# Kernel optimization log

Measured on AMD Instinct MI355X. Metric: run time of the kernel, lower is better.

Reference implementation:

```python
import jax, jax.numpy as jnp
import numpy as np

B, C, W, H = 16, 256, 32, 32  # L = W*H = 1024
NUM_HEAD = 4
DIM_HEAD = C  # dim_head defaults to in_channels


def setup_inputs() -> dict:
    key = jax.random.key(0)
    ks = jax.random.split(key, 6)
    s = 0.02  # small init scale, like trained linear weights
    return {
        "x": jax.random.normal(ks[0], (B, C, W, H), dtype=jnp.float32),
        "Wq": jax.random.normal(ks[1], (NUM_HEAD, DIM_HEAD, C), dtype=jnp.float32) * s,
        "Wk": jax.random.normal(ks[2], (NUM_HEAD, DIM_HEAD, C), dtype=jnp.float32) * s,
        "Wv": jax.random.normal(ks[3], (NUM_HEAD, DIM_HEAD, C), dtype=jnp.float32) * s,
        "Wo_w": jax.random.normal(ks[4], (C, NUM_HEAD * DIM_HEAD), dtype=jnp.float32) * s,
        "Wo_b": jax.random.normal(ks[5], (C,), dtype=jnp.float32) * s,
    }


def reference(x, Wq, Wk, Wv, Wo_w, Wo_b):
    b, c, w, h = x.shape
    L = w * h
    # [b,c,w,h] -> [b,L,c]
    xs = jnp.transpose(x, (0, 2, 3, 1)).reshape(b, L, c)
    # per-head projections (torch Linear: y = x @ W^T), batched over heads
    Q = jnp.einsum('blc,hdc->bhld', xs, Wq)
    K = jnp.einsum('blc,hdc->bhld', xs, Wk)
    V = jnp.einsum('blc,hdc->bhld', xs, Wv)
    # no softmax: scores = Q K^T, heads = scores V
    scores = jnp.einsum('bhld,bhmd->bhlm', Q, K)  # [b,H,L,L]
    heads = jnp.einsum('bhlm,bhmd->bhld', scores, V)  # [b,H,L,d]
    # concat heads along channel dim -> [b,L,H*d], then output projection
    cat = jnp.transpose(heads, (0, 2, 1, 3)).reshape(b, L, -1)
    z = cat @ Wo_w.T + Wo_b  # [b,L,c]
    return jnp.transpose(z, (0, 2, 1)).reshape(b, c, w, h)
```

## Files before the change

kernel.cpp:

```cpp
#include <hip/hip_runtime.h>
#include <hip/hip_bf16.h>

typedef __attribute__((ext_vector_type(8))) short s8v;
typedef __attribute__((ext_vector_type(4))) float f4v;

__device__ inline ushort f2bf(float f) {
    unsigned u = __builtin_bit_cast(unsigned, f);
    unsigned r = (u + 0x7fffu + ((u >> 16) & 1u)) >> 16;
    return (ushort)r;
}

__device__ inline void gload16(const ushort* g, ushort* l) {
    __builtin_amdgcn_global_load_lds(
        (const __attribute__((address_space(1))) unsigned*)g,
        (__attribute__((address_space(3))) unsigned*)l, 16, 0, 0);
}

__global__ __launch_bounds__(256) void kprep(
    const float* __restrict__ x, const float* __restrict__ Wq, const float* __restrict__ Wk,
    const float* __restrict__ Wv, const float* __restrict__ Wo,
    ushort* __restrict__ xb, ushort* __restrict__ xlc,
    ushort* __restrict__ wqT, ushort* __restrict__ wkT, ushort* __restrict__ wvT,
    ushort* __restrict__ wo16) {
    __shared__ __align__(16) ushort t[64][72];
    int j = blockIdx.x, tid = threadIdx.x;
    int r = tid >> 2, c0 = (tid & 3) * 16;
    if (j < 1024) {
        int lt = j & 15, ct = (j >> 4) & 3, b = j >> 6;
        size_t so = ((size_t)(b * 256 + ct * 64 + r)) * 1024 + lt * 64 + c0;
        const float* src = x + so;
        ushort* db = xb + so;
#pragma unroll
        for (int i = 0; i < 16; i += 4) {
            float4 v = *(const float4*)(src + i);
            ushort4 u = { f2bf(v.x), f2bf(v.y), f2bf(v.z), f2bf(v.w) };
            *(ushort4*)(db + i) = u;
            *(ushort4*)(&t[r][c0 + i]) = u;
        }
        __syncthreads();
        ushort* dl = xlc + ((size_t)(b * 1024 + lt * 64 + r)) * 256 + ct * 64 + c0;
#pragma unroll
        for (int i = 0; i < 16; i += 4) {
            ushort4 u = { t[c0 + i][r], t[c0 + i + 1][r], t[c0 + i + 2][r], t[c0 + i + 3][r] };
            *(ushort4*)(dl + i) = u;
        }
    } else if (j < 1216) {
        int q = j - 1024;
        int tile = q & 15, h = (q >> 4) & 3, which = q >> 6;
        const float* src = which == 0 ? Wq : which == 1 ? Wk : Wv;
        ushort* dst = which == 0 ? wqT : which == 1 ? wkT : wvT;
        int tr = tile >> 2, tc = tile & 3;
        const float* s = src + (size_t)h * 65536 + (size_t)(tr * 64 + r) * 256 + tc * 64 + c0;
#pragma unroll
        for (int i = 0; i < 16; i += 4) {
            float4 v = *(const float4*)(s + i);
            ushort4 u = { f2bf(v.x), f2bf(v.y), f2bf(v.z), f2bf(v.w) };
            *(ushort4*)(&t[r][c0 + i]) = u;
        }
        __syncthreads();
        ushort* d = dst + (size_t)h * 65536 + (size_t)(tc * 64 + r) * 256 + tr * 64 + c0;
#pragma unroll
        for (int i = 0; i < 16; i += 4) {
            ushort4 u = { t[c0 + i][r], t[c0 + i + 1][r], t[c0 + i + 2][r], t[c0 + i + 3][r] };
            *(ushort4*)(d + i) = u;
        }
    } else {
        int q = j - 1216;
#pragma unroll
        for (int rr = 0; rr < 4; ++rr) {
            int i = (q * 1024 + rr * 256 + tid) * 4;
            float4 v = *(const float4*)(Wo + i);
            ushort4 u = { f2bf(v.x), f2bf(v.y), f2bf(v.z), f2bf(v.w) };
            *(ushort4*)(wo16 + i) = u;
        }
    }
}


__device__ __forceinline__ void gemm64p(
    const ushort* __restrict__ Xb, const ushort* __restrict__ Yb,
    int ldx, int ldy, ushort* lds, int row0, int col0, int K,
    ushort* __restrict__ O, int ldo) {
    const int tid = threadIdx.x, wave = tid >> 6, lane = tid & 63;
    const int wr = wave >> 1, wc = wave & 1;
    const int rA = lane & 15, kg = lane >> 4;
    const int srow = wave * 16 + (lane >> 2);
    const int scol = ((lane & 3) ^ ((lane >> 3) & 3)) * 8;
    ushort* LA = lds;
    ushort* LB = lds + 8192;
    const int NT = K >> 5;
    f4v acc[2][2] = {};

    const ushort* gx = Xb + (size_t)(row0 + srow) * ldx + scol;
    const ushort* gy = Yb + (size_t)(col0 + srow) * ldy + scol;
    gload16(gx + 0,  LA + 0 * 2048 + wave * 512);
    gload16(gy + 0,  LB + 0 * 2048 + wave * 512);
    gload16(gx + 32, LA + 1 * 2048 + wave * 512);
    gload16(gy + 32, LB + 1 * 2048 + wave * 512);

    for (int t = 0; t < NT; ++t) {
        if (t + 2 < NT) {
            int s2 = (t + 2) & 3, kt = (t + 2) << 5;
            gload16(gx + kt, LA + s2 * 2048 + wave * 512);
            gload16(gy + kt, LB + s2 * 2048 + wave * 512);
            asm volatile("s_waitcnt vmcnt(4)" ::: "memory");
        } else if (t + 1 < NT) {
            asm volatile("s_waitcnt vmcnt(2)" ::: "memory");
        } else {
            asm volatile("s_waitcnt vmcnt(0)" ::: "memory");
        }
        __builtin_amdgcn_s_barrier();
        __builtin_amdgcn_sched_barrier(0);
        const int s = t & 3;
        const ushort* pa = LA + s * 2048;
        const ushort* pb = LB + s * 2048;
        s8v a[2], b[2];
#pragma unroll
        for (int m = 0; m < 2; ++m) {
            int row = wr * 32 + m * 16 + rA;
            a[m] = *(const s8v*)&pa[row * 32 + ((kg ^ ((row >> 1) & 3)) << 3)];
        }
#pragma unroll
        for (int n = 0; n < 2; ++n) {
            int row = wc * 32 + n * 16 + rA;
            b[n] = *(const s8v*)&pb[row * 32 + ((kg ^ ((row >> 1) & 3)) << 3)];
        }
#pragma unroll
        for (int m = 0; m < 2; ++m)
#pragma unroll
            for (int n = 0; n < 2; ++n)
                acc[m][n] = __builtin_amdgcn_mfma_f32_16x16x32_bf16(a[m], b[n], acc[m][n], 0, 0, 0);
    }

    int r4 = (lane >> 4) * 4, cl = lane & 15;
#pragma unroll
    for (int m = 0; m < 2; ++m)
#pragma unroll
        for (int n = 0; n < 2; ++n) {
            int row = row0 + wr * 32 + m * 16 + r4;
            int col = col0 + wc * 32 + n * 16 + cl;
#pragma unroll
            for (int r = 0; r < 4; ++r)
                O[(size_t)(row + r) * ldo + col] = f2bf(acc[m][n][r]);
        }
}

template<int OBF>
__device__ __forceinline__ void gemm128p(
    const ushort* __restrict__ Xb, const ushort* __restrict__ Yb,
    int ldx, int ldy, ushort* lds, int row0, int col0, int K,
    void* __restrict__ Oraw, int ldo, const float* __restrict__ bias) {
    const int tid = threadIdx.x, wave = tid >> 6, lane = tid & 63;
    const int wr = wave >> 1, wc = wave & 1;
    const int rA = lane & 15, kg = lane >> 4;
    const int sr = lane >> 2;
    const int scol = ((lane & 3) ^ ((lane >> 3) & 3)) * 8;
    ushort* LA = lds;
    ushort* LB = lds + 16384;
    const int NT = K >> 5;
    f4v acc[4][4] = {};

    const int ch0 = wave, ch1 = 4 + wave;
    const ushort* gx0 = Xb + (size_t)(row0 + ch0 * 16 + sr) * ldx + scol;
    const ushort* gx1 = Xb + (size_t)(row0 + ch1 * 16 + sr) * ldx + scol;
    const ushort* gy0 = Yb + (size_t)(col0 + ch0 * 16 + sr) * ldy + scol;
    const ushort* gy1 = Yb + (size_t)(col0 + ch1 * 16 + sr) * ldy + scol;

#pragma unroll
    for (int p = 0; p < 2; ++p) {
        int kt = p << 5;
        gload16(gx0 + kt, LA + p * 4096 + ch0 * 512);
        gload16(gx1 + kt, LA + p * 4096 + ch1 * 512);
        gload16(gy0 + kt, LB + p * 4096 + ch0 * 512);
        gload16(gy1 + kt, LB + p * 4096 + ch1 * 512);
    }

    for (int t = 0; t < NT; ++t) {
        if (t + 2 < NT) {
            int s2 = (t + 2) & 3, kt = (t + 2) << 5;
            gload16(gx0 + kt, LA + s2 * 4096 + ch0 * 512);
            gload16(gx1 + kt, LA + s2 * 4096 + ch1 * 512);
            gload16(gy0 + kt, LB + s2 * 4096 + ch0 * 512);
            gload16(gy1 + kt, LB + s2 * 4096 + ch1 * 512);
            asm volatile("s_waitcnt vmcnt(8)" ::: "memory");
        } else if (t + 1 < NT) {
            asm volatile("s_waitcnt vmcnt(4)" ::: "memory");
        } else {
            asm volatile("s_waitcnt vmcnt(0)" ::: "memory");
        }
        __builtin_amdgcn_s_barrier();
        __builtin_amdgcn_sched_barrier(0);
        const int s = t & 3;
        const ushort* pa = LA + s * 4096;
        const ushort* pb = LB + s * 4096;
        s8v a[4], b[4];
#pragma unroll
        for (int m = 0; m < 4; ++m) {
            int row = wr * 64 + m * 16 + rA;
            a[m] = *(const s8v*)&pa[row * 32 + ((kg ^ ((row >> 1) & 3)) << 3)];
        }
#pragma unroll
        for (int n = 0; n < 4; ++n) {
            int row = wc * 64 + n * 16 + rA;
            b[n] = *(const s8v*)&pb[row * 32 + ((kg ^ ((row >> 1) & 3)) << 3)];
        }
#pragma unroll
        for (int m = 0; m < 4; ++m)
#pragma unroll
            for (int n = 0; n < 4; ++n)
                acc[m][n] = __builtin_amdgcn_mfma_f32_16x16x32_bf16(a[m], b[n], acc[m][n], 0, 0, 0);
    }

    int r4 = (lane >> 4) * 4, cl = lane & 15;
    if (OBF) {
        ushort* O = (ushort*)Oraw;
#pragma unroll
        for (int m = 0; m < 4; ++m)
#pragma unroll
            for (int n = 0; n < 4; ++n) {
                int row = row0 + wr * 64 + m * 16 + r4;
                int col = col0 + wc * 64 + n * 16 + cl;
#pragma unroll
                for (int r = 0; r < 4; ++r)
                    O[(size_t)(row + r) * ldo + col] = f2bf(acc[m][n][r]);
            }
    } else {
        float* O = (float*)Oraw;
#pragma unroll
        for (int m = 0; m < 4; ++m)
#pragma unroll
            for (int n = 0; n < 4; ++n) {
                int row = row0 + wr * 64 + m * 16 + r4;
                int col = col0 + wc * 64 + n * 16 + cl;
#pragma unroll
                for (int r = 0; r < 4; ++r) {
                    float bv = bias ? bias[row + r] : 0.f;
                    O[(size_t)(row + r) * ldo + col] = acc[m][n][r] + bv;
                }
            }
    }
}

__global__ __launch_bounds__(256) void k2_sa(
    const ushort* __restrict__ xb, const ushort* __restrict__ wqT, const ushort* __restrict__ wkT,
    const ushort* __restrict__ wo16, const ushort* __restrict__ wvT,
    ushort* __restrict__ S16, ushort* __restrict__ A16, ushort* __restrict__ BT) {
    __shared__ __align__(16) ushort lds[32768];
    int j = blockIdx.x;
    if (j < 256) {
        int xcd = j & 7, idx = j >> 3;
        int b = 2 * xcd + (idx >> 4), tile = idx & 15;
        int tm = tile >> 2, tn = tile & 3;
        const ushort* Xb = xb + (size_t)b * 262144;
        gemm64p(Xb, Xb, 1024, 1024, lds, tm * 64, tn * 64, 1024,
                S16 + (size_t)b * 65536, 256);
    } else {
        int q = j - 256;
        if (q < 16) {
            int h = q >> 2, tm = (q >> 1) & 1, tn = q & 1;
            gemm128p<1>(wqT + h * 65536, wkT + h * 65536, 256, 256, lds,
                        tm * 128, tn * 128, 256, A16 + h * 65536, 256, nullptr);
        } else {
            q -= 16;
            int h = q >> 2, tm = (q >> 1) & 1, tn = q & 1;
            gemm128p<1>(wo16 + h * 256, wvT + h * 65536, 1024, 256, lds,
                        tm * 128, tn * 128, 256, BT + h * 256, 1024, nullptr);
        }
    }
}

__global__ __launch_bounds__(256) void k3_t1(
    const ushort* __restrict__ A16, const ushort* __restrict__ S16,
    ushort* __restrict__ T1) {
    __shared__ __align__(16) ushort lds[32768];
    int j = blockIdx.x;
    int xcd = j & 7, idx = j >> 3;
    int b = 2 * xcd + (idx >> 4), h = (idx >> 2) & 3, tile = idx & 3;
    int tm = tile >> 1, tn = tile & 1;
    gemm128p<1>(A16 + h * 65536, S16 + (size_t)b * 65536, 256, 256, lds,
                tm * 128, tn * 128, 256, T1 + (size_t)b * 262144 + h * 256, 1024, nullptr);
}

__global__ __launch_bounds__(256) void k4_gt(
    const ushort* __restrict__ BT, const ushort* __restrict__ T1, ushort* __restrict__ GT) {
    __shared__ __align__(16) ushort lds[16384];
    int j = blockIdx.x;
    int xcd = j & 7, idx = j >> 3;
    int b = 2 * xcd + (idx >> 4), tile = idx & 15;
    int tm = tile >> 2, tn = tile & 3;
    gemm64p(BT, T1 + (size_t)b * 262144, 1024, 1024, lds, tm * 64, tn * 64, 1024,
            GT + (size_t)b * 65536, 256);
}

__global__ __launch_bounds__(256) void k5_out(
    const ushort* __restrict__ GT, const ushort* __restrict__ xlc,
    float* __restrict__ out, const float* __restrict__ bias) {
    __shared__ __align__(16) ushort lds[32768];
    int j = blockIdx.x;
    int xcd = j & 7, idx = j >> 3;
    int b = 2 * xcd + (idx >> 4), tile = idx & 15;
    int tm = tile >> 3, tn = tile & 7;
    gemm128p<0>(GT + (size_t)b * 65536, xlc + (size_t)b * 262144, 256, 256, lds,
                tm * 128, tn * 128, 256, out + (size_t)b * 262144, 1024, bias);
}

extern "C" void kernel_launch(void* const* d_in, const int* in_sizes, int n_in,
                              void* d_out, int out_size, void* d_ws, size_t ws_size,
                              hipStream_t stream) {
    const float* x  = (const float*)d_in[0];
    const float* Wq = (const float*)d_in[1];
    const float* Wk = (const float*)d_in[2];
    const float* Wv = (const float*)d_in[3];
    const float* Wo = (const float*)d_in[4];
    const float* Wb = (const float*)d_in[5];

    char* ws = (char*)d_ws;
    ushort* xb   = (ushort*)(ws + 0);
    ushort* xlc  = (ushort*)(ws + 8388608);
    ushort* wqT  = (ushort*)(ws + 16777216);
    ushort* wkT  = (ushort*)(ws + 17301504);
    ushort* wvT  = (ushort*)(ws + 17825792);
    ushort* wo16 = (ushort*)(ws + 18350080);
    ushort* A16  = (ushort*)(ws + 18874368);
    ushort* BT   = (ushort*)(ws + 19398656);
    ushort* S16  = (ushort*)(ws + 19922944);
    ushort* GT   = (ushort*)(ws + 22020096);
    ushort* T1   = xb;

    hipLaunchKernelGGL(kprep, dim3(1280), dim3(256), 0, stream,
                       x, Wq, Wk, Wv, Wo, xb, xlc, wqT, wkT, wvT, wo16);
    hipLaunchKernelGGL(k2_sa, dim3(288), dim3(256), 0, stream,
                       xb, wqT, wkT, wo16, wvT, S16, A16, BT);
    hipLaunchKernelGGL(k3_t1, dim3(256), dim3(256), 0, stream, A16, S16, T1);
    hipLaunchKernelGGL(k4_gt, dim3(256), dim3(256), 0, stream, BT, T1, GT);
    hipLaunchKernelGGL(k5_out, dim3(256), dim3(256), 0, stream, GT, xlc, (float*)d_out, Wb);
}
```

Baseline: 46.57 us.

## Fuse five stages into one cooperative persistent kernel with 512-thread split-K blocks

Replaces the five separate launches with a single cooperative kernel of 256 blocks of 512 threads that runs the prep, S/A/B, T1, GT and output stages separated by grid-wide syncs. The goal is to remove per-launch overhead and tail gaps between kernels. The 64x64 GEMMs are now split along K across two 4-wave groups and reduced through LDS, and the 128x128 GEMMs spread their tile over 8 waves, to keep each larger block busy. Grid syncs add their own cost, the single-pass prep now loops over more tiles per block, and the old multi-kernel path remains as a fallback if the cooperative launch fails.

```diff
diff --git a/kernel.cpp b/kernel.cpp
--- a/kernel.cpp
+++ b/kernel.cpp
@@ -1,108 +1,107 @@
 #include <hip/hip_runtime.h>
 #include <hip/hip_bf16.h>
+#include <hip/hip_cooperative_groups.h>
+
+namespace cg = cooperative_groups;
 
 typedef __attribute__((ext_vector_type(8))) short s8v;
 typedef __attribute__((ext_vector_type(4))) float f4v;
 
-__device__ inline ushort f2bf(float f) {
+__device__ __forceinline__ ushort f2bf(float f) {
     unsigned u = __builtin_bit_cast(unsigned, f);
     unsigned r = (u + 0x7fffu + ((u >> 16) & 1u)) >> 16;
     return (ushort)r;
 }
 
-__device__ inline void gload16(const ushort* g, ushort* l) {
+__device__ __forceinline__ void gload16(const ushort* g, ushort* l) {
     __builtin_amdgcn_global_load_lds(
         (const __attribute__((address_space(1))) unsigned*)g,
         (__attribute__((address_space(3))) unsigned*)l, 16, 0, 0);
 }
 
-__global__ __launch_bounds__(256) void kprep(
-    const float* __restrict__ x, const float* __restrict__ Wq, const float* __restrict__ Wk,
-    const float* __restrict__ Wv, const float* __restrict__ Wo,
-    ushort* __restrict__ xb, ushort* __restrict__ xlc,
-    ushort* __restrict__ wqT, ushort* __restrict__ wkT, ushort* __restrict__ wvT,
-    ushort* __restrict__ wo16) {
-    __shared__ __align__(16) ushort t[64][72];
-    int j = blockIdx.x, tid = threadIdx.x;
-    int r = tid >> 2, c0 = (tid & 3) * 16;
-    if (j < 1024) {
-        int lt = j & 15, ct = (j >> 4) & 3, b = j >> 6;
-        size_t so = ((size_t)(b * 256 + ct * 64 + r)) * 1024 + lt * 64 + c0;
-        const float* src = x + so;
-        ushort* db = xb + so;
-#pragma unroll
-        for (int i = 0; i < 16; i += 4) {
-            float4 v = *(const float4*)(src + i);
-            ushort4 u = { f2bf(v.x), f2bf(v.y), f2bf(v.z), f2bf(v.w) };
-            *(ushort4*)(db + i) = u;
-            *(ushort4*)(&t[r][c0 + i]) = u;
-        }
+__device__ __forceinline__ void stageP(
+    ushort* lds, const float* x, const float* Wq, const float* Wk, const float* Wv,
+    const float* Wo, ushort* xb, ushort* xlc, ushort* wqT, ushort* wkT, ushort* wvT,
+    ushort* wo16) {
+    ushort (*t)[72] = (ushort(*)[72])lds;
+    int tid = threadIdx.x;
+    int r = tid >> 3, c0 = (tid & 7) * 8;
+    for (int j = blockIdx.x; j < 1280; j += 256) {
         __syncthreads();
-        ushort* dl = xlc + ((size_t)(b * 1024 + lt * 64 + r)) * 256 + ct * 64 + c0;
-#pragma unroll
-        for (int i = 0; i < 16; i += 4) {
-            ushort4 u = { t[c0 + i][r], t[c0 + i + 1][r], t[c0 + i + 2][r], t[c0 + i + 3][r] };
-            *(ushort4*)(dl + i) = u;
-        }
-    } else if (j < 1216) {
-        int q = j - 1024;
-        int tile = q & 15, h = (q >> 4) & 3, which = q >> 6;
-        const float* src = which == 0 ? Wq : which == 1 ? Wk : Wv;
-        ushort* dst = which == 0 ? wqT : which == 1 ? wkT : wvT;
-        int tr = tile >> 2, tc = tile & 3;
-        const float* s = src + (size_t)h * 65536 + (size_t)(tr * 64 + r) * 256 + tc * 64 + c0;
-#pragma unroll
-        for (int i = 0; i < 16; i += 4) {
-            float4 v = *(const float4*)(s + i);
-            ushort4 u = { f2bf(v.x), f2bf(v.y), f2bf(v.z), f2bf(v.w) };
-            *(ushort4*)(&t[r][c0 + i]) = u;
-        }
-        __syncthreads();
-        ushort* d = dst + (size_t)h * 65536 + (size_t)(tc * 64 + r) * 256 + tr * 64 + c0;
-#pragma unroll
-        for (int i = 0; i < 16; i += 4) {
-            ushort4 u = { t[c0 + i][r], t[c0 + i + 1][r], t[c0 + i + 2][r], t[c0 + i + 3][r] };
-            *(ushort4*)(d + i) = u;
-        }
-    } else {
-        int q = j - 1216;
-#pragma unroll
-        for (int rr = 0; rr < 4; ++rr) {
-            int i = (q * 1024 + rr * 256 + tid) * 4;
-            float4 v = *(const float4*)(Wo + i);
-            ushort4 u = { f2bf(v.x), f2bf(v.y), f2bf(v.z), f2bf(v.w) };
-            *(ushort4*)(wo16 + i) = u;
-        }
-    }
-}
-
-
-__device__ __forceinline__ void gemm64p(
-    const ushort* __restrict__ Xb, const ushort* __restrict__ Yb,
-    int ldx, int ldy, ushort* lds, int row0, int col0, int K,
-    ushort* __restrict__ O, int ldo) {
+        if (j < 1024) {
+            int lt = j & 15, ct = (j >> 4) & 3, b = j >> 6;
+            size_t so = ((size_t)(b * 256 + ct * 64 + r)) * 1024 + lt * 64 + c0;
+            float4 v0 = *(const float4*)(x + so);
+            float4 v1 = *(const float4*)(x + so + 4);
+            ushort4 u0 = { f2bf(v0.x), f2bf(v0.y), f2bf(v0.z), f2bf(v0.w) };
+            ushort4 u1 = { f2bf(v1.x), f2bf(v1.y), f2bf(v1.z), f2bf(v1.w) };
+            *(ushort4*)(xb + so) = u0;
+            *(ushort4*)(xb + so + 4) = u1;
+            *(ushort4*)&t[r][c0] = u0;
+            *(ushort4*)&t[r][c0 + 4] = u1;
+            __syncthreads();
+            size_t dof = ((size_t)(b * 1024 + lt * 64 + r)) * 256 + ct * 64 + c0;
+            ushort4 w0 = { t[c0][r], t[c0 + 1][r], t[c0 + 2][r], t[c0 + 3][r] };
+            ushort4 w1 = { t[c0 + 4][r], t[c0 + 5][r], t[c0 + 6][r], t[c0 + 7][r] };
+            *(ushort4*)(xlc + dof) = w0;
+            *(ushort4*)(xlc + dof + 4) = w1;
+        } else if (j < 1216) {
+            int q = j - 1024;
+            int tile = q & 15, h = (q >> 4) & 3, which = q >> 6;
+            const float* src = which == 0 ? Wq : which == 1 ? Wk : Wv;
+            ushort* dst = which == 0 ? wqT : which == 1 ? wkT : wvT;
+            int tr = tile >> 2, tc = tile & 3;
+            const float* s = src + (size_t)h * 65536 + (size_t)(tr * 64 + r) * 256 + tc * 64 + c0;
+            float4 v0 = *(const float4*)(s);
+            float4 v1 = *(const float4*)(s + 4);
+            ushort4 u0 = { f2bf(v0.x), f2bf(v0.y), f2bf(v0.z), f2bf(v0.w) };
+            ushort4 u1 = { f2bf(v1.x), f2bf(v1.y), f2bf(v1.z), f2bf(v1.w) };
+            *(ushort4*)&t[r][c0] = u0;
+            *(ushort4*)&t[r][c0 + 4] = u1;
+            __syncthreads();
+            ushort* d = dst + (size_t)h * 65536 + (size_t)(tc * 64 + r) * 256 + tr * 64 + c0;
+            ushort4 w0 = { t[c0][r], t[c0 + 1][r], t[c0 + 2][r], t[c0 + 3][r] };
+            ushort4 w1 = { t[c0 + 4][r], t[c0 + 5][r], t[c0 + 6][r], t[c0 + 7][r] };
+            *(ushort4*)(d) = w0;
+            *(ushort4*)(d + 4) = w1;
+        } else {
+            int q = j - 1216;
+            size_t i = (size_t)q * 4096 + (size_t)tid * 8;
+            float4 v0 = *(const float4*)(Wo + i);
+            float4 v1 = *(const float4*)(Wo + i + 4);
+            ushort4 u0 = { f2bf(v0.x), f2bf(v0.y), f2bf(v0.z), f2bf(v0.w) };
+            ushort4 u1 = { f2bf(v1.x), f2bf(v1.y), f2bf(v1.z), f2bf(v1.w) };
+            *(ushort4*)(wo16 + i) = u0;
+            *(ushort4*)(wo16 + i + 4) = u1;
+        }
+    }
+}
+
+__device__ __forceinline__ void gemm64x8(
+    const ushort* Xb, const ushort* Yb, int ldx, int ldy, ushort* lds,
+    int row0, int col0, int K, ushort* O, int ldo) {
     const int tid = threadIdx.x, wave = tid >> 6, lane = tid & 63;
-    const int wr = wave >> 1, wc = wave & 1;
+    const int g = wave >> 2, w4 = wave & 3;
+    const int wr = w4 >> 1, wc = w4 & 1;
     const int rA = lane & 15, kg = lane >> 4;
-    const int srow = wave * 16 + (lane >> 2);
+    const int srow = w4 * 16 + (lane >> 2);
     const int scol = ((lane & 3) ^ ((lane >> 3) & 3)) * 8;
-    ushort* LA = lds;
-    ushort* LB = lds + 8192;
-    const int NT = K >> 5;
+    const int K2 = K >> 1, NT = K2 >> 5, kb = g * K2;
+    ushort* LA = lds + g * 16384;
+    ushort* LB = LA + 8192;
     f4v acc[2][2] = {};
-
-    const ushort* gx = Xb + (size_t)(row0 + srow) * ldx + scol;
-    const ushort* gy = Yb + (size_t)(col0 + srow) * ldy + scol;
-    gload16(gx + 0,  LA + 0 * 2048 + wave * 512);
-    gload16(gy + 0,  LB + 0 * 2048 + wave * 512);
-    gload16(gx + 32, LA + 1 * 2048 + wave * 512);
-    gload16(gy + 32, LB + 1 * 2048 + wave * 512);
-
+    __syncthreads();
+    const ushort* gx = Xb + (size_t)(row0 + srow) * ldx + kb + scol;
+    const ushort* gy = Yb + (size_t)(col0 + srow) * ldy + kb + scol;
+    gload16(gx,      LA + w4 * 512);
+    gload16(gy,      LB + w4 * 512);
+    gload16(gx + 32, LA + 2048 + w4 * 512);
+    gload16(gy + 32, LB + 2048 + w4 * 512);
     for (int t = 0; t < NT; ++t) {
         if (t + 2 < NT) {
             int s2 = (t + 2) & 3, kt = (t + 2) << 5;
-            gload16(gx + kt, LA + s2 * 2048 + wave * 512);
-            gload16(gy + kt, LB + s2 * 2048 + wave * 512);
+            gload16(gx + kt, LA + s2 * 2048 + w4 * 512);
+            gload16(gy + kt, LB + s2 * 2048 + w4 * 512);
             asm volatile("s_waitcnt vmcnt(4)" ::: "memory");
         } else if (t + 1 < NT) {
             asm volatile("s_waitcnt vmcnt(2)" ::: "memory");
@@ -111,9 +110,8 @@
         }
         __builtin_amdgcn_s_barrier();
         __builtin_amdgcn_sched_barrier(0);
-        const int s = t & 3;
-        const ushort* pa = LA + s * 2048;
-        const ushort* pb = LB + s * 2048;
+        const ushort* pa = LA + (t & 3) * 2048;
+        const ushort* pb = LB + (t & 3) * 2048;
         s8v a[2], b[2];
 #pragma unroll
         for (int m = 0; m < 2; ++m) {
@@ -131,95 +129,95 @@
             for (int n = 0; n < 2; ++n)
                 acc[m][n] = __builtin_amdgcn_mfma_f32_16x16x32_bf16(a[m], b[n], acc[m][n], 0, 0, 0);
     }
-
-    int r4 = (lane >> 4) * 4, cl = lane & 15;
-#pragma unroll
-    for (int m = 0; m < 2; ++m)
-#pragma unroll
-        for (int n = 0; n < 2; ++n) {
-            int row = row0 + wr * 32 + m * 16 + r4;
-            int col = col0 + wc * 32 + n * 16 + cl;
-#pragma unroll
-            for (int r = 0; r < 4; ++r)
-                O[(size_t)(row + r) * ldo + col] = f2bf(acc[m][n][r]);
-        }
+    __syncthreads();
+    float* red = (float*)lds;
+    if (g == 1) {
+#pragma unroll
+        for (int m = 0; m < 2; ++m)
+#pragma unroll
+            for (int n = 0; n < 2; ++n)
+                *(f4v*)&red[(w4 * 64 + lane) * 16 + (m * 2 + n) * 4] = acc[m][n];
+    }
+    __syncthreads();
+    if (g == 0) {
+        int r4 = (lane >> 4) * 4, cl = lane & 15;
+#pragma unroll
+        for (int m = 0; m < 2; ++m)
+#pragma unroll
+            for (int n = 0; n < 2; ++n) {
+                f4v o = *(const f4v*)&red[(w4 * 64 + lane) * 16 + (m * 2 + n) * 4];
+                f4v s = acc[m][n] + o;
+                int row = row0 + wr * 32 + m * 16 + r4;
+                int col = col0 + wc * 32 + n * 16 + cl;
+#pragma unroll
+                for (int r = 0; r < 4; ++r)
+                    O[(size_t)(row + r) * ldo + col] = f2bf(s[r]);
+            }
+    }
 }
 
 template<int OBF>
-__device__ __forceinline__ void gemm128p(
-    const ushort* __restrict__ Xb, const ushort* __restrict__ Yb,
-    int ldx, int ldy, ushort* lds, int row0, int col0, int K,
-    void* __restrict__ Oraw, int ldo, const float* __restrict__ bias) {
+__device__ __forceinline__ void gemm128x8(
+    const ushort* Xb, const ushort* Yb, int ldx, int ldy, ushort* lds,
+    int row0, int col0, int K, void* Oraw, int ldo, const float* bias) {
     const int tid = threadIdx.x, wave = tid >> 6, lane = tid & 63;
-    const int wr = wave >> 1, wc = wave & 1;
+    const int wr = wave >> 2, wc = wave & 3;
     const int rA = lane & 15, kg = lane >> 4;
     const int sr = lane >> 2;
     const int scol = ((lane & 3) ^ ((lane >> 3) & 3)) * 8;
+    const int NT = K >> 5;
     ushort* LA = lds;
     ushort* LB = lds + 16384;
-    const int NT = K >> 5;
-    f4v acc[4][4] = {};
-
-    const int ch0 = wave, ch1 = 4 + wave;
-    const ushort* gx0 = Xb + (size_t)(row0 + ch0 * 16 + sr) * ldx + scol;
-    const ushort* gx1 = Xb + (size_t)(row0 + ch1 * 16 + sr) * ldx + scol;
-    const ushort* gy0 = Yb + (size_t)(col0 + ch0 * 16 + sr) * ldy + scol;
-    const ushort* gy1 = Yb + (size_t)(col0 + ch1 * 16 + sr) * ldy + scol;
-
+    f4v acc[4][2] = {};
+    __syncthreads();
+    const ushort* gx = Xb + (size_t)(row0 + wave * 16 + sr) * ldx + scol;
+    const ushort* gy = Yb + (size_t)(col0 + wave * 16 + sr) * ldy + scol;
 #pragma unroll
     for (int p = 0; p < 2; ++p) {
-        int kt = p << 5;
-        gload16(gx0 + kt, LA + p * 4096 + ch0 * 512);
-        gload16(gx1 + kt, LA + p * 4096 + ch1 * 512);
-        gload16(gy0 + kt, LB + p * 4096 + ch0 * 512);
-        gload16(gy1 + kt, LB + p * 4096 + ch1 * 512);
-    }
-
+        gload16(gx + p * 32, LA + p * 4096 + wave * 512);
+        gload16(gy + p * 32, LB + p * 4096 + wave * 512);
+    }
     for (int t = 0; t < NT; ++t) {
         if (t + 2 < NT) {
             int s2 = (t + 2) & 3, kt = (t + 2) << 5;
-            gload16(gx0 + kt, LA + s2 * 4096 + ch0 * 512);
-            gload16(gx1 + kt, LA + s2 * 4096 + ch1 * 512);
-            gload16(gy0 + kt, LB + s2 * 4096 + ch0 * 512);
-            gload16(gy1 + kt, LB + s2 * 4096 + ch1 * 512);
-            asm volatile("s_waitcnt vmcnt(8)" ::: "memory");
+            gload16(gx + kt, LA + s2 * 4096 + wave * 512);
+            gload16(gy + kt, LB + s2 * 4096 + wave * 512);
+            asm volatile("s_waitcnt vmcnt(4)" ::: "memory");
         } else if (t + 1 < NT) {
-            asm volatile("s_waitcnt vmcnt(4)" ::: "memory");
+            asm volatile("s_waitcnt vmcnt(2)" ::: "memory");
         } else {
             asm volatile("s_waitcnt vmcnt(0)" ::: "memory");
         }
         __builtin_amdgcn_s_barrier();
         __builtin_amdgcn_sched_barrier(0);
-        const int s = t & 3;
-        const ushort* pa = LA + s * 4096;
-        const ushort* pb = LB + s * 4096;
-        s8v a[4], b[4];
+        const ushort* pa = LA + (t & 3) * 4096;
+        const ushort* pb = LB + (t & 3) * 4096;
+        s8v a[4], b[2];
 #pragma unroll
         for (int m = 0; m < 4; ++m) {
             int row = wr * 64 + m * 16 + rA;
             a[m] = *(const s8v*)&pa[row * 32 + ((kg ^ ((row >> 1) & 3)) << 3)];
         }
 #pragma unroll
-        for (int n = 0; n < 4; ++n) {
-            int row = wc * 64 + n * 16 + rA;
+        for (int n = 0; n < 2; ++n) {
+            int row = wc * 32 + n * 16 + rA;
             b[n] = *(const s8v*)&pb[row * 32 + ((kg ^ ((row >> 1) & 3)) << 3)];
         }
 #pragma unroll
         for (int m = 0; m < 4; ++m)
 #pragma unroll
-            for (int n = 0; n < 4; ++n)
+            for (int n = 0; n < 2; ++n)
                 acc[m][n] = __builtin_amdgcn_mfma_f32_16x16x32_bf16(a[m], b[n], acc[m][n], 0, 0, 0);
     }
-
     int r4 = (lane >> 4) * 4, cl = lane & 15;
     if (OBF) {
         ushort* O = (ushort*)Oraw;
 #pragma unroll
         for (int m = 0; m < 4; ++m)
 #pragma unroll
-            for (int n = 0; n < 4; ++n) {
+            for (int n = 0; n < 2; ++n) {
                 int row = row0 + wr * 64 + m * 16 + r4;
-                int col = col0 + wc * 64 + n * 16 + cl;
+                int col = col0 + wc * 32 + n * 16 + cl;
 #pragma unroll
                 for (int r = 0; r < 4; ++r)
                     O[(size_t)(row + r) * ldo + col] = f2bf(acc[m][n][r]);
@@ -229,79 +227,107 @@
 #pragma unroll
         for (int m = 0; m < 4; ++m)
 #pragma unroll
-            for (int n = 0; n < 4; ++n) {
+            for (int n = 0; n < 2; ++n) {
                 int row = row0 + wr * 64 + m * 16 + r4;
-                int col = col0 + wc * 64 + n * 16 + cl;
-#pragma unroll
-                for (int r = 0; r < 4; ++r) {
-                    float bv = bias ? bias[row + r] : 0.f;
-                    O[(size_t)(row + r) * ldo + col] = acc[m][n][r] + bv;
-                }
+                int col = col0 + wc * 32 + n * 16 + cl;
+#pragma unroll
+                for (int r = 0; r < 4; ++r)
+                    O[(size_t)(row + r) * ldo + col] = acc[m][n][r] + bias[row + r];
             }
     }
 }
 
-__global__ __launch_bounds__(256) void k2_sa(
-    const ushort* __restrict__ xb, const ushort* __restrict__ wqT, const ushort* __restrict__ wkT,
-    const ushort* __restrict__ wo16, const ushort* __restrict__ wvT,
-    ushort* __restrict__ S16, ushort* __restrict__ A16, ushort* __restrict__ BT) {
-    __shared__ __align__(16) ushort lds[32768];
+__device__ __forceinline__ void stageSA(
+    ushort* lds, const ushort* xb, const ushort* wqT, const ushort* wkT,
+    const ushort* wo16, const ushort* wvT, ushort* S16, ushort* A16, ushort* BT) {
     int j = blockIdx.x;
-    if (j < 256) {
-        int xcd = j & 7, idx = j >> 3;
-        int b = 2 * xcd + (idx >> 4), tile = idx & 15;
-        int tm = tile >> 2, tn = tile & 3;
-        const ushort* Xb = xb + (size_t)b * 262144;
-        gemm64p(Xb, Xb, 1024, 1024, lds, tm * 64, tn * 64, 1024,
-                S16 + (size_t)b * 65536, 256);
-    } else {
-        int q = j - 256;
-        if (q < 16) {
-            int h = q >> 2, tm = (q >> 1) & 1, tn = q & 1;
-            gemm128p<1>(wqT + h * 65536, wkT + h * 65536, 256, 256, lds,
-                        tm * 128, tn * 128, 256, A16 + h * 65536, 256, nullptr);
-        } else {
-            q -= 16;
-            int h = q >> 2, tm = (q >> 1) & 1, tn = q & 1;
-            gemm128p<1>(wo16 + h * 256, wvT + h * 65536, 1024, 256, lds,
-                        tm * 128, tn * 128, 256, BT + h * 256, 1024, nullptr);
-        }
-    }
-}
-
-__global__ __launch_bounds__(256) void k3_t1(
-    const ushort* __restrict__ A16, const ushort* __restrict__ S16,
-    ushort* __restrict__ T1) {
-    __shared__ __align__(16) ushort lds[32768];
+    int xcd = j & 7, idx = j >> 3;
+    int b = 2 * xcd + (idx >> 4), tile = idx & 15;
+    const ushort* Xb = xb + (size_t)b * 262144;
+    gemm64x8(Xb, Xb, 1024, 1024, lds, (tile >> 2) * 64, (tile & 3) * 64, 1024,
+             S16 + (size_t)b * 65536, 256);
+    if (j < 128) {
+        int which = j >> 6, q = j & 63, h = q >> 4, t2 = q & 15;
+        if (which == 0)
+            gemm64x8(wqT + h * 65536, wkT + h * 65536, 256, 256, lds,
+                     (t2 >> 2) * 64, (t2 & 3) * 64, 256, A16 + h * 65536, 256);
+        else
+            gemm64x8(wo16 + h * 256, wvT + h * 65536, 1024, 256, lds,
+                     (t2 >> 2) * 64, (t2 & 3) * 64, 256, BT + h * 256, 1024);
+    }
+}
+
+__device__ __forceinline__ void stageT1(
+    ushort* lds, const ushort* A16, const ushort* S16, ushort* T1) {
     int j = blockIdx.x;
     int xcd = j & 7, idx = j >> 3;
     int b = 2 * xcd + (idx >> 4), h = (idx >> 2) & 3, tile = idx & 3;
-    int tm = tile >> 1, tn = tile & 1;
-    gemm128p<1>(A16 + h * 65536, S16 + (size_t)b * 65536, 256, 256, lds,
-                tm * 128, tn * 128, 256, T1 + (size_t)b * 262144 + h * 256, 1024, nullptr);
-}
-
-__global__ __launch_bounds__(256) void k4_gt(
-    const ushort* __restrict__ BT, const ushort* __restrict__ T1, ushort* __restrict__ GT) {
-    __shared__ __align__(16) ushort lds[16384];
+    gemm128x8<1>(A16 + h * 65536, S16 + (size_t)b * 65536, 256, 256, lds,
+                 (tile >> 1) * 128, (tile & 1) * 128, 256,
+                 T1 + (size_t)b * 262144 + h * 256, 1024, nullptr);
+}
+
+__device__ __forceinline__ void stageGT(
+    ushort* lds, const ushort* BT, const ushort* T1, ushort* GT) {
     int j = blockIdx.x;
     int xcd = j & 7, idx = j >> 3;
     int b = 2 * xcd + (idx >> 4), tile = idx & 15;
-    int tm = tile >> 2, tn = tile & 3;
-    gemm64p(BT, T1 + (size_t)b * 262144, 1024, 1024, lds, tm * 64, tn * 64, 1024,
-            GT + (size_t)b * 65536, 256);
-}
-
-__global__ __launch_bounds__(256) void k5_out(
-    const ushort* __restrict__ GT, const ushort* __restrict__ xlc,
-    float* __restrict__ out, const float* __restrict__ bias) {
-    __shared__ __align__(16) ushort lds[32768];
+    gemm64x8(BT, T1 + (size_t)b * 262144, 1024, 1024, lds,
+             (tile >> 2) * 64, (tile & 3) * 64, 1024, GT + (size_t)b * 65536, 256);
+}
+
+__device__ __forceinline__ void stageOUT(
+    ushort* lds, const ushort* GT, const ushort* xlc, float* out, const float* bias) {
     int j = blockIdx.x;
     int xcd = j & 7, idx = j >> 3;
     int b = 2 * xcd + (idx >> 4), tile = idx & 15;
-    int tm = tile >> 3, tn = tile & 7;
-    gemm128p<0>(GT + (size_t)b * 65536, xlc + (size_t)b * 262144, 256, 256, lds,
-                tm * 128, tn * 128, 256, out + (size_t)b * 262144, 1024, bias);
+    gemm128x8<0>(GT + (size_t)b * 65536, xlc + (size_t)b * 262144, 256, 256, lds,
+                 (tile >> 3) * 128, (tile & 7) * 128, 256,
+                 out + (size_t)b * 262144, 1024, bias);
+}
+
+__global__ __launch_bounds__(512, 2) void mega(
+    const float* __restrict__ x, const float* __restrict__ Wq, const float* __restrict__ Wk,
+    const float* __restrict__ Wv, const float* __restrict__ Wo, const float* __restrict__ Wb,
+    float* __restrict__ out, ushort* xb, ushort* xlc, ushort* wqT, ushort* wkT,
+    ushort* wvT, ushort* wo16, ushort* A16, ushort* BT, ushort* S16, ushort* GT) {
+    __shared__ __align__(16) ushort lds[32768];
+    cg::grid_group grid = cg::this_grid();
+    stageP(lds, x, Wq, Wk, Wv, Wo, xb, xlc, wqT, wkT, wvT, wo16);
+    grid.sync();
+    stageSA(lds, xb, wqT, wkT, wo16, wvT, S16, A16, BT);
+    grid.sync();
+    stageT1(lds, A16, S16, xb);
+    grid.sync();
+    stageGT(lds, BT, xb, GT);
+    grid.sync();
+    stageOUT(lds, GT, xlc, out, Wb);
+}
+
+__global__ __launch_bounds__(512, 2) void kP(
+    const float* x, const float* Wq, const float* Wk, const float* Wv, const float* Wo,
+    ushort* xb, ushort* xlc, ushort* wqT, ushort* wkT, ushort* wvT, ushort* wo16) {
+    __shared__ __align__(16) ushort lds[32768];
+    stageP(lds, x, Wq, Wk, Wv, Wo, xb, xlc, wqT, wkT, wvT, wo16);
+}
+__global__ __launch_bounds__(512, 2) void kSA(
+    const ushort* xb, const ushort* wqT, const ushort* wkT, const ushort* wo16,
+    const ushort* wvT, ushort* S16, ushort* A16, ushort* BT) {
+    __shared__ __align__(16) ushort lds[32768];
+    stageSA(lds, xb, wqT, wkT, wo16, wvT, S16, A16, BT);
+}
+__global__ __launch_bounds__(512, 2) void kT1(const ushort* A16, const ushort* S16, ushort* T1) {
+    __shared__ __align__(16) ushort lds[32768];
+    stageT1(lds, A16, S16, T1);
+}
+__global__ __launch_bounds__(512, 2) void kGT(const ushort* BT, const ushort* T1, ushort* GT) {
+    __shared__ __align__(16) ushort lds[32768];
+    stageGT(lds, BT, T1, GT);
+}
+__global__ __launch_bounds__(512, 2) void kOUT(
+    const ushort* GT, const ushort* xlc, float* out, const float* bias) {
+    __shared__ __align__(16) ushort lds[32768];
+    stageOUT(lds, GT, xlc, out, bias);
 }
 
 extern "C" void kernel_launch(void* const* d_in, const int* in_sizes, int n_in,
@@ -313,6 +339,7 @@
     const float* Wv = (const float*)d_in[3];
     const float* Wo = (const float*)d_in[4];
     const float* Wb = (const float*)d_in[5];
+    float* outp = (float*)d_out;
 
     char* ws = (char*)d_ws;
     ushort* xb   = (ushort*)(ws + 0);
@@ -325,13 +352,19 @@
     ushort* BT   = (ushort*)(ws + 19398656);
     ushort* S16  = (ushort*)(ws + 19922944);
     ushort* GT   = (ushort*)(ws + 22020096);
-    ushort* T1   = xb;
-
-    hipLaunchKernelGGL(kprep, dim3(1280), dim3(256), 0, stream,
-                       x, Wq, Wk, Wv, Wo, xb, xlc, wqT, wkT, wvT, wo16);
-    hipLaunchKernelGGL(k2_sa, dim3(288), dim3(256), 0, stream,
-                       xb, wqT, wkT, wo16, wvT, S16, A16, BT);
-    hipLaunchKernelGGL(k3_t1, dim3(256), dim3(256), 0, stream, A16, S16, T1);
-    hipLaunchKernelGGL(k4_gt, dim3(256), dim3(256), 0, stream, BT, T1, GT);
-    hipLaunchKernelGGL(k5_out, dim3(256), dim3(256), 0, stream, GT, xlc, (float*)d_out, Wb);
-}
+
+    void* args[] = { &x, &Wq, &Wk, &Wv, &Wo, &Wb, &outp, &xb, &xlc, &wqT, &wkT,
+                     &wvT, &wo16, &A16, &BT, &S16, &GT };
+    hipError_t e = hipLaunchCooperativeKernel((void*)mega, dim3(256), dim3(512),
+                                              args, 0, stream);
+    if (e != hipSuccess) {
+        (void)hipGetLastError();
+        hipLaunchKernelGGL(kP,  dim3(256), dim3(512), 0, stream,
+                           x, Wq, Wk, Wv, Wo, xb, xlc, wqT, wkT, wvT, wo16);
+        hipLaunchKernelGGL(kSA, dim3(256), dim3(512), 0, stream,
+                           xb, wqT, wkT, wo16, wvT, S16, A16, BT);
+        hipLaunchKernelGGL(kT1, dim3(256), dim3(512), 0, stream, A16, S16, xb);
+        hipLaunchKernelGGL(kGT, dim3(256), dim3(512), 0, stream, BT, xb, GT);
+        hipLaunchKernelGGL(kOUT, dim3(256), dim3(512), 0, stream, GT, xlc, outp, Wb);
+    }
+}
```

Result: slower. 170.4 us (+265.9%).
